# Kernel tuning notes

Hardware: AMD Instinct MI355X
Metric: run time of the kernel (lower is better)

## Reference

```python
import jax, jax.numpy as jnp
import numpy as np

B, C, S = 32, 64, 112
RATIO = 8
EPS = 1e-5


def conv1x1(x, w, b):
    # 1x1 conv == channel-mixing matmul. x:[B,C,H,W], w:[O,C], b:[O]
    return jnp.einsum('oc,bchw->bohw', w, x) + b[None, :, None, None]


def dwconv(x, w, b):
    # grouped 1x1 conv with groups=C: per-channel scale + bias
    return x * w[None, :, None, None] + b[None, :, None, None]


def bn(x, g, b):
    # BatchNorm2d in training mode: batch stats over (N,H,W), biased var
    m = x.mean((0, 2, 3), keepdims=True)
    v = x.var((0, 2, 3), keepdims=True)
    return (x - m) * jax.lax.rsqrt(v + EPS) * g[None, :, None, None] + b[None, :, None, None]


def avgpool(x, k):
    # nn.AvgPool2d(k): kernel k, stride k, VALID (floor) padding
    s = jax.lax.reduce_window(x, 0.0, jax.lax.add, (1, 1, k, k), (1, 1, k, k), 'VALID')
    return s / float(k * k)


def setup_inputs() -> dict:
    key = jax.random.key(0)
    ks = jax.random.split(key, 20)
    C2, H = 2 * C, (2 * C) // RATIO

    def n(k, shape, s=0.02):
        return jax.random.normal(k, shape, jnp.float32) * s

    return {
        'rgb': jax.random.normal(ks[0], (B, C, S, S), jnp.float32),
        'fre': jax.random.normal(ks[1], (B, C, S, S), jnp.float32),
        'wq_fad': n(ks[2], (C, C)), 'bq_fad': jnp.zeros((C,), jnp.float32),
        'wq_lfs': n(ks[3], (C, C)), 'bq_lfs': jnp.zeros((C,), jnp.float32),
        'wk_fad': n(ks[4], (C, C)), 'bk_fad': jnp.zeros((C,), jnp.float32),
        'wk_lfs': n(ks[5], (C, C)), 'bk_lfs': jnp.zeros((C,), jnp.float32),
        'fad_gamma': n(ks[6], (1,), 1.0), 'lfs_gamma': n(ks[7], (1,), 1.0),
        'fad_cw': n(ks[8], (C,), 1.0), 'fad_cb': jnp.zeros((C,), jnp.float32),
        'fad_bg': jnp.ones((C,), jnp.float32), 'fad_bb': jnp.zeros((C,), jnp.float32),
        'lfs_cw': n(ks[9], (C,), 1.0), 'lfs_cb': jnp.zeros((C,), jnp.float32),
        'lfs_bg': jnp.ones((C,), jnp.float32), 'lfs_bb': jnp.zeros((C,), jnp.float32),
        'lin1_w': n(ks[10], (3,), 0.3), 'lin2_w': n(ks[11], (3,), 0.3),
        'mlp_w1': n(ks[12], (H, C2)), 'mlp_w2': n(ks[13], (C2, H)),
        'rgb_cw': n(ks[14], (C,), 1.0), 'rgb_cb': jnp.zeros((C,), jnp.float32),
        'rgb_bg': jnp.ones((C,), jnp.float32), 'rgb_bb': jnp.zeros((C,), jnp.float32),
        'fre_cw': n(ks[15], (C,), 1.0), 'fre_cb': jnp.zeros((C,), jnp.float32),
        'fre_bg': jnp.ones((C,), jnp.float32), 'fre_bb': jnp.zeros((C,), jnp.float32),
    }


def reference(rgb, fre, wq_fad, bq_fad, wq_lfs, bq_lfs, wk_fad, bk_fad, wk_lfs, bk_lfs,
              fad_gamma, lfs_gamma, fad_cw, fad_cb, fad_bg, fad_bb,
              lfs_cw, lfs_cb, lfs_bg, lfs_bb, lin1_w, lin2_w, mlp_w1, mlp_w2,
              rgb_cw, rgb_cb, rgb_bg, rgb_bb, fre_cw, fre_cb, fre_bg, fre_bb):
    Bn, Cn, Sz, _ = rgb.shape
    # ---- MixBlock: cross attention over folded (B*C) batch ----
    qF = conv1x1(rgb, wq_fad, bq_fad).reshape(Bn * Cn, Sz, Sz)
    qL = conv1x1(fre, wq_lfs, bq_lfs).reshape(Bn * Cn, Sz, Sz)
    Mq = jnp.concatenate([qF, qL], axis=2)          # [BC, S, 2S]
    kF = conv1x1(rgb, wk_fad, bk_fad).reshape(Bn * Cn, Sz, Sz).transpose(0, 2, 1)
    kL = conv1x1(fre, wk_lfs, bk_lfs).reshape(Bn * Cn, Sz, Sz).transpose(0, 2, 1)
    Mk = jnp.concatenate([kF, kL], axis=1)          # [BC, 2S, S]
    attn = jax.nn.softmax(jnp.matmul(Mq, Mk), axis=-1).reshape(Bn, Cn, Sz, Sz)
    att_lfs = fre * attn * (jax.nn.sigmoid(lfs_gamma) * 2.0 - 1.0)
    y_fad = rgb + bn(dwconv(att_lfs, fad_cw, fad_cb), fad_bg, fad_bb)
    att_fad = rgb * attn * (jax.nn.sigmoid(fad_gamma) * 2.0 - 1.0)
    y_lfs = fre + bn(dwconv(att_fad, lfs_cw, lfs_cb), lfs_bg, lfs_bb)
    # ---- MSCA on concatenated channels ----
    x = jnp.concatenate([y_fad, y_lfs], axis=1)     # [B, 2C, S, S]
    avgs, maxs = [], []
    for k in (3, 5, 7):
        m = avgpool(x, k)
        avgs.append(m.mean((2, 3)))
        maxs.append(m.max((2, 3)))
    a_p = jnp.stack(avgs, -1) @ lin1_w              # [B, 2C]
    m_p = jnp.stack(maxs, -1) @ lin2_w

    def mlp(v):
        h = jax.nn.relu(jnp.einsum('rc,bc->br', mlp_w1, v))
        return jnp.einsum('cr,br->bc', mlp_w2, h)

    ca = jax.nn.sigmoid(mlp(a_p) + mlp(m_p))        # [B, 2C]
    r_c = ca[:, :Cn, None, None]
    f_c = ca[:, Cn:, None, None]
    rgb_out = y_fad + bn(dwconv(r_c * y_fad, rgb_cw, rgb_cb), rgb_bg, rgb_bb)
    fre_out = y_lfs + bn(dwconv(f_c * y_lfs, fre_cw, fre_cb), fre_bg, fre_bb)
    return (rgb_out, fre_out)
```

## Files before the change

kernel.cpp:

```cpp
#include <hip/hip_runtime.h>
#include <hip/hip_bf16.h>
#include <stdint.h>

#define NE 25690112ull
#define PP 12544
#define SS 112
#define EPSV 1e-5f

typedef __attribute__((ext_vector_type(8))) short short8v;
typedef __attribute__((ext_vector_type(4))) float float4v;

__device__ __forceinline__ unsigned short f2bf(float x){
  union { __hip_bfloat16 h; unsigned short u; } cv;
  cv.h = __float2bfloat16(x);
  return cv.u;
}
__device__ __forceinline__ ushort4 f2bf4(float a, float b, float c, float d){
  union { __hip_bfloat162 h2[2]; ushort4 u; } cv;
  cv.h2[0] = __float22bfloat162_rn(make_float2(a, b));
  cv.h2[1] = __float22bfloat162_rn(make_float2(c, d));
  return cv.u;
}
__device__ __forceinline__ float bf2f(unsigned short u){ return __uint_as_float(((uint32_t)u) << 16); }

__global__ __launch_bounds__(256) void k1_conv(
    const float* __restrict__ rgb, const float* __restrict__ fre,
    const float* __restrict__ wq_fad, const float* __restrict__ bq_fad,
    const float* __restrict__ wk_fad, const float* __restrict__ bk_fad,
    const float* __restrict__ wq_lfs, const float* __restrict__ bq_lfs,
    const float* __restrict__ wk_lfs, const float* __restrict__ bk_lfs,
    unsigned short* __restrict__ qF, unsigned short* __restrict__ kF,
    unsigned short* __restrict__ qL, unsigned short* __restrict__ kL)
{
  const int bx = blockIdx.x, b = blockIdx.y, z = blockIdx.z;
  const float* X  = z ? fre : rgb;
  const float* Wq = z ? wq_lfs : wq_fad;
  const float* Bq = z ? bq_lfs : bq_fad;
  const float* Wk = z ? wk_lfs : wk_fad;
  const float* Bk = z ? bk_lfs : bk_fad;
  unsigned short* Oq = z ? qL : qF;
  unsigned short* Ok = z ? kL : kF;

  __shared__ __align__(16) unsigned short xs[256 * 64];

  const int tid = threadIdx.x, lane = tid & 63, w = tid >> 6;
  const int lc = lane & 15, l4 = lane >> 4;

  const int p0 = bx*256;
  const size_t xbase = (size_t)b * 64 * PP;
  const int c0 = (tid & 15) * 4;
  const int pq = (tid >> 4) * 4;
  #pragma unroll
  for (int itp = 0; itp < 4; ++itp){
    const int p = itp*64 + pq;
    float4 xr[4];
    #pragma unroll
    for (int k = 0; k < 4; ++k)
      xr[k] = *(const float4*)(X + xbase + (size_t)(c0+k)*PP + p0 + p);
    const float* v0 = &xr[0].x;
    const float* v1 = &xr[1].x;
    const float* v2 = &xr[2].x;
    const float* v3 = &xr[3].x;
    #pragma unroll
    for (int j = 0; j < 4; ++j){
      ushort4 t = f2bf4(v0[j], v1[j], v2[j], v3[j]);
      uint32_t byteS = (uint32_t)((p+j)*128 + c0*2) ^ (uint32_t)(((p+j) & 7) << 4);
      *(ushort4*)((char*)xs + byteS) = t;
    }
  }
  __syncthreads();

  short8v afr[4][2];
  #pragma unroll
  for (int t = 0; t < 4; ++t){
    const int row = (t*4 + w)*16 + lc;
    const uint32_t rbase = (uint32_t)(row*128);
    const uint32_t sw = (uint32_t)((row & 7) << 4);
    afr[t][0] = *(const short8v*)((const char*)xs + ((rbase + l4*16) ^ sw));
    afr[t][1] = *(const short8v*)((const char*)xs + ((rbase + 64 + l4*16) ^ sw));
  }
  __syncthreads();

  #pragma unroll
  for (int arr = 0; arr < 2; ++arr){
    const float* W = arr ? Wk : Wq;
    const float* Bi = arr ? Bk : Bq;
    unsigned short* O = arr ? Ok : Oq;
    short8v wf[4][2];
    float bias[4];
    #pragma unroll
    for (int ot = 0; ot < 4; ++ot){
      bias[ot] = Bi[ot*16 + lc];
      #pragma unroll
      for (int ks = 0; ks < 2; ++ks){
        const int base = (ot*16 + lc)*64 + ks*32 + l4*8;
        const float4 q0 = *(const float4*)(W + base);
        const float4 q1 = *(const float4*)(W + base + 4);
        union { ushort4 u[2]; short8v v; } pk;
        pk.u[0] = f2bf4(q0.x, q0.y, q0.z, q0.w);
        pk.u[1] = f2bf4(q1.x, q1.y, q1.z, q1.w);
        wf[ot][ks] = pk.v;
      }
    }
    #pragma unroll
    for (int t = 0; t < 4; ++t){
      const int pt = (t*4 + w)*16;
      #pragma unroll
      for (int ot = 0; ot < 4; ++ot){
        float4v acc = (float4v){bias[ot], bias[ot], bias[ot], bias[ot]};
        acc = __builtin_amdgcn_mfma_f32_16x16x32_bf16(afr[t][0], wf[ot][0], acc, 0, 0, 0);
        acc = __builtin_amdgcn_mfma_f32_16x16x32_bf16(afr[t][1], wf[ot][1], acc, 0, 0, 0);
        ushort4 u = f2bf4(acc[0], acc[1], acc[2], acc[3]);
        const int o = ot*16 + lc;
        uint32_t byteS = (uint32_t)(o*512 + (pt + l4*4)*2) ^ (uint32_t)((o & 7) << 4);
        *(ushort4*)((char*)xs + byteS) = u;
      }
    }
    __syncthreads();
    for (int i = tid; i < 2048; i += 256){
      const int o = i >> 5, s = i & 31;
      uint32_t byteS = (uint32_t)(o*512 + s*16) ^ (uint32_t)((o & 7) << 4);
      short8v v = *(const short8v*)((const char*)xs + byteS);
      *(short8v*)(O + ((size_t)b*64 + o)*PP + p0 + s*8) = v;
    }
    __syncthreads();
  }
}

__global__ __launch_bounds__(448) void k2_attn(
    unsigned short* __restrict__ qF, const unsigned short* __restrict__ qL,
    const unsigned short* __restrict__ kF, const unsigned short* __restrict__ kL,
    const float* __restrict__ rgb, const float* __restrict__ fre,
    const float* __restrict__ fad_gamma, const float* __restrict__ lfs_gamma,
    float* __restrict__ stats)
{
  const int bc = blockIdx.x, c = bc & 63;
  const size_t plane = (size_t)bc * PP;
  __shared__ __align__(16) unsigned short ksF[PP + 16];
  __shared__ __align__(16) unsigned short ksL[PP + 16];
  const int tid = threadIdx.x, lane = tid & 63, w = tid >> 6;
  const int l4 = lane >> 4, lc = lane & 15;

  const unsigned short* qFp = qF + plane;
  const unsigned short* qLp = qL + plane;
  const int qrow = w*16 + lc;
  short8v aF[4], aL[4];
  #pragma unroll
  for (int ks = 0; ks < 4; ++ks){
    const int joff = ks*32 + l4*8;
    if ((ks < 3) || (l4 < 2)){
      aF[ks] = *(const short8v*)(qFp + qrow*SS + joff);
      aL[ks] = *(const short8v*)(qLp + qrow*SS + joff);
    } else {
      aF[ks] = (short8v)(short)0;
      aL[ks] = (short8v)(short)0;
    }
  }

  const uint32_t* kFu = (const uint32_t*)kF + plane/2;
  const uint32_t* kLu = (const uint32_t*)kL + plane/2;
  uint32_t* ksFw = (uint32_t*)ksF;
  uint32_t* ksLw = (uint32_t*)ksL;
  #pragma unroll
  for (int t = 0; t < 14; ++t){
    const int i = tid + t*448;
    ksFw[i] = kFu[i];
    ksLw[i] = kLu[i];
  }
  __syncthreads();

  float4v acc[7];
  #pragma unroll
  for (int ct = 0; ct < 7; ++ct) acc[ct] = (float4v)0.f;
  #pragma unroll
  for (int ks = 0; ks < 4; ++ks){
    #pragma unroll
    for (int ct = 0; ct < 7; ++ct){
      const uint32_t off = (uint32_t)((ct*16 + lc)*224 + ks*64 + l4*16);
      short8v bF = *(const short8v*)((const char*)ksF + off);
      short8v bL = *(const short8v*)((const char*)ksL + off);
      acc[ct] = __builtin_amdgcn_mfma_f32_16x16x32_bf16(aF[ks], bF, acc[ct], 0, 0, 0);
      acc[ct] = __builtin_amdgcn_mfma_f32_16x16x32_bf16(aL[ks], bL, acc[ct], 0, 0, 0);
    }
  }

  const float sF = 2.f/(1.f + __expf(-fad_gamma[0])) - 1.f;
  const float sL = 2.f/(1.f + __expf(-lfs_gamma[0])) - 1.f;
  unsigned short* attnP = qF + plane;
  unsigned short* alin = ksF;

  __syncthreads();
  #pragma unroll
  for (int r = 0; r < 4; ++r){
    const int i = w*16 + l4*4 + r;
    float v[7];
    #pragma unroll
    for (int ct = 0; ct < 7; ++ct) v[ct] = acc[ct][r];
    float m = fmaxf(fmaxf(fmaxf(v[0],v[1]),fmaxf(v[2],v[3])), fmaxf(fmaxf(v[4],v[5]),v[6]));
    #pragma unroll
    for (int off = 8; off; off >>= 1) m = fmaxf(m, __shfl_xor(m, off, 64));
    float e[7]; float s = 0.f;
    #pragma unroll
    for (int ct = 0; ct < 7; ++ct){ e[ct] = __expf(v[ct] - m); s += e[ct]; }
    #pragma unroll
    for (int off = 8; off; off >>= 1) s += __shfl_xor(s, off, 64);
    const float inv = 1.f / s;
    #pragma unroll
    for (int ct = 0; ct < 7; ++ct)
      alin[i*SS + ct*16 + lc] = f2bf(e[ct] * inv);
  }
  __syncthreads();

  float ls1 = 0.f, lq1 = 0.f, ls2 = 0.f, lq2 = 0.f;
  #pragma unroll
  for (int t = 0; t < 7; ++t){
    const int i4 = tid + t*448;
    ushort4 av = *(const ushort4*)(alin + i4*4);
    *(ushort4*)(attnP + (size_t)i4*4) = av;
    float4 fr = *(const float4*)(fre + plane + (size_t)i4*4);
    float4 rg = *(const float4*)(rgb + plane + (size_t)i4*4);
    const unsigned short* ap = &av.x;
    const float fp[4] = {fr.x, fr.y, fr.z, fr.w};
    const float rp[4] = {rg.x, rg.y, rg.z, rg.w};
    #pragma unroll
    for (int j = 0; j < 4; ++j){
      float a = bf2f(ap[j]);
      float v1 = fp[j] * a * sL;
      float v2 = rp[j] * a * sF;
      ls1 += v1; lq1 += v1*v1; ls2 += v2; lq2 += v2*v2;
    }
  }
  #pragma unroll
  for (int off = 32; off; off >>= 1){
    ls1 += __shfl_xor(ls1, off, 64);
    lq1 += __shfl_xor(lq1, off, 64);
    ls2 += __shfl_xor(ls2, off, 64);
    lq2 += __shfl_xor(lq2, off, 64);
  }
  if (lane == 0){
    atomicAdd(&stats[c],       ls1);
    atomicAdd(&stats[64 + c],  lq1);
    atomicAdd(&stats[128 + c], ls2);
    atomicAdd(&stats[192 + c], lq2);
  }
}

__global__ void k3_affine1(const float* __restrict__ stats,
    const float* __restrict__ fad_cw, const float* __restrict__ fad_bg, const float* __restrict__ fad_bb,
    const float* __restrict__ lfs_cw, const float* __restrict__ lfs_bg, const float* __restrict__ lfs_bb,
    float* __restrict__ AB)
{
  int c = threadIdx.x;
  if (c >= 64) return;
  const float n = 401408.f;
  {
    float m1 = stats[c]/n, v1 = stats[64+c]/n - (stats[c]/n)*(stats[c]/n);
    float cw = fad_cw[c], g = fad_bg[c];
    float rs = rsqrtf(cw*cw*v1 + EPSV);
    AB[c]      = cw*rs*g;
    AB[64 + c] = -cw*m1*rs*g + fad_bb[c];
  }
  {
    float m2 = stats[128+c]/n, v2 = stats[192+c]/n - (stats[128+c]/n)*(stats[128+c]/n);
    float cw = lfs_cw[c], g = lfs_bg[c];
    float rs = rsqrtf(cw*cw*v2 + EPSV);
    AB[128 + c] = cw*rs*g;
    AB[192 + c] = -cw*m2*rs*g + lfs_bb[c];
  }
}

__global__ __launch_bounds__(512) void k4_fuse(
    const unsigned short* __restrict__ attn,
    const float* __restrict__ rgb, const float* __restrict__ fre,
    const float* __restrict__ AB1,
    const float* __restrict__ fad_gamma, const float* __restrict__ lfs_gamma,
    float* __restrict__ avgstat, float* __restrict__ maxstat,
    float4* __restrict__ planeStats)
{
  const int bc = blockIdx.x, b = bc >> 6, c = bc & 63;
  const size_t plane = (size_t)bc * PP;
  __shared__ unsigned short ys[2][112][113];
  __shared__ float redA[8][4];
  __shared__ float redS[8], redM[8];
  const int tid = threadIdx.x, lane = tid & 63, w = tid >> 6;
  const float sF = 2.f/(1.f + __expf(-fad_gamma[0])) - 1.f;
  const float sL = 2.f/(1.f + __expf(-lfs_gamma[0])) - 1.f;
  const float A1 = AB1[c], B1 = AB1[64+c], A2 = AB1[128+c], B2 = AB1[192+c];
  float s0 = 0.f, q0 = 0.f, s1 = 0.f, q1 = 0.f;

  for (int i4 = tid; i4 < 3136; i4 += 512){
    ushort4 av = *(const ushort4*)(attn + plane + (size_t)i4*4);
    float4 rg = *(const float4*)(rgb + plane + (size_t)i4*4);
    float4 fr = *(const float4*)(fre + plane + (size_t)i4*4);
    float aa[4] = {bf2f(av.x), bf2f(av.y), bf2f(av.z), bf2f(av.w)};
    float rr[4] = {rg.x, rg.y, rg.z, rg.w};
    float ff[4] = {fr.x, fr.y, fr.z, fr.w};
    int r = i4 / 28, c0 = (i4 % 28) * 4;
    float y0[4], y1[4];
    #pragma unroll
    for (int j = 0; j < 4; ++j){
      float t1 = ff[j]*aa[j]*sL;
      float t2 = rr[j]*aa[j]*sF;
      y0[j] = rr[j] + A1*t1 + B1;
      y1[j] = ff[j] + A2*t2 + B2;
      s0 += y0[j]; q0 += y0[j]*y0[j];
      s1 += y1[j]; q1 += y1[j]*y1[j];
    }
    *(ushort4*)(&ys[0][r][c0]) = f2bf4(y0[0], y0[1], y0[2], y0[3]);
    *(ushort4*)(&ys[1][r][c0]) = f2bf4(y1[0], y1[1], y1[2], y1[3]);
  }
  #pragma unroll
  for (int off = 32; off; off >>= 1){
    s0 += __shfl_xor(s0, off, 64); q0 += __shfl_xor(q0, off, 64);
    s1 += __shfl_xor(s1, off, 64); q1 += __shfl_xor(q1, off, 64);
  }
  if (lane == 0){ redA[w][0] = s0; redA[w][1] = q0; redA[w][2] = s1; redA[w][3] = q1; }
  __syncthreads();
  if (tid == 0){
    float a0=0,a1=0,a2=0,a3=0;
    for (int i = 0; i < 8; ++i){ a0+=redA[i][0]; a1+=redA[i][1]; a2+=redA[i][2]; a3+=redA[i][3]; }
    float4 ps = {a0,a1,a2,a3};
    planeStats[bc] = ps;
  }
  __syncthreads();

  const int kk[3] = {3,5,7};
  const int gg[3] = {37,22,16};
  for (int pl = 0; pl < 2; ++pl){
    const int cc = pl*64 + c;
    for (int ki = 0; ki < 3; ++ki){
      const int k = kk[ki], g = gg[ki];
      float sumAll = 0.f, mx = -3.0e38f;
      for (int win = tid; win < g*g; win += 512){
        int wy = win / g, wx = win % g;
        float s = 0.f;
        for (int dy = 0; dy < k; ++dy)
          for (int dx = 0; dx < k; ++dx)
            s += bf2f(ys[pl][wy*k+dy][wx*k+dx]);
        sumAll += s; mx = fmaxf(mx, s);
      }
      #pragma unroll
      for (int off = 32; off; off >>= 1){
        sumAll += __shfl_xor(sumAll, off, 64);
        mx = fmaxf(mx, __shfl_xor(mx, off, 64));
      }
      if (lane == 0){ redS[w] = sumAll; redM[w] = mx; }
      __syncthreads();
      if (tid == 0){
        float st = 0.f, mt = -3.0e38f;
        for (int i = 0; i < 8; ++i){ st += redS[i]; mt = fmaxf(mt, redM[i]); }
        int idx = (b*128 + cc)*3 + ki;
        avgstat[idx] = st / (float)(k*k*g*g);
        maxstat[idx] = mt / (float)(k*k);
      }
      __syncthreads();
    }
  }
}

__global__ void k6_mlp(const float* __restrict__ avgstat, const float* __restrict__ maxstat,
    const float* __restrict__ lin1, const float* __restrict__ lin2,
    const float* __restrict__ w1, const float* __restrict__ w2,
    float* __restrict__ ca)
{
  const int b = blockIdx.x, tid = threadIdx.x;
  __shared__ float sa[128], sm[128], hA[16], hM[16];
  int idx = (b*128 + tid)*3;
  sa[tid] = avgstat[idx]*lin1[0] + avgstat[idx+1]*lin1[1] + avgstat[idx+2]*lin1[2];
  sm[tid] = maxstat[idx]*lin2[0] + maxstat[idx+1]*lin2[1] + maxstat[idx+2]*lin2[2];
  __syncthreads();
  if (tid < 16){
    float ha = 0.f, hm = 0.f;
    for (int c2 = 0; c2 < 128; ++c2){
      ha += w1[tid*128 + c2]*sa[c2];
      hm += w1[tid*128 + c2]*sm[c2];
    }
    hA[tid] = fmaxf(ha, 0.f); hM[tid] = fmaxf(hm, 0.f);
  }
  __syncthreads();
  float o = 0.f;
  for (int r = 0; r < 16; ++r) o += w2[tid*16 + r]*(hA[r] + hM[r]);
  ca[b*128 + tid] = 1.f/(1.f + __expf(-o));
}

__global__ void k8_affineF(const float4* __restrict__ planeStats, const float* __restrict__ ca,
    const float* __restrict__ rgb_cw, const float* __restrict__ rgb_bg, const float* __restrict__ rgb_bb,
    const float* __restrict__ fre_cw, const float* __restrict__ fre_bg, const float* __restrict__ fre_bb,
    float* __restrict__ ABF)
{
  int t = threadIdx.x;
  if (t >= 128) return;
  int z = t >> 6, c = t & 63;
  float S = 0.f, Q = 0.f;
  for (int b = 0; b < 32; ++b){
    float4 ps = planeStats[b*64 + c];
    float sc = ca[b*128 + t];
    float sp = z ? ps.z : ps.x;
    float qp = z ? ps.w : ps.y;
    S += sc*sp; Q += sc*sc*qp;
  }
  const float n = 401408.f;
  float m = S/n, v = Q/n - m*m;
  float cw = z ? fre_cw[c] : rgb_cw[c];
  float g  = z ? fre_bg[c] : rgb_bg[c];
  float bb = z ? fre_bb[c] : rgb_bb[c];
  float rs = rsqrtf(cw*cw*v + EPSV);
  ABF[z*128 + c]      = cw*rs*g;
  ABF[z*128 + 64 + c] = -cw*m*rs*g + bb;
}

__global__ __launch_bounds__(256) void k9_out(
    const unsigned short* __restrict__ attn,
    const float* __restrict__ rgb, const float* __restrict__ fre,
    const float* __restrict__ AB1,
    const float* __restrict__ fad_gamma, const float* __restrict__ lfs_gamma,
    const float* __restrict__ ca, const float* __restrict__ ABF,
    float* __restrict__ out)
{
  const int c = blockIdx.x, b = blockIdx.y;
  const size_t plane = ((size_t)b*64 + c)*PP;
  const float sF = 2.f/(1.f + __expf(-fad_gamma[0])) - 1.f;
  const float sL = 2.f/(1.f + __expf(-lfs_gamma[0])) - 1.f;
  const float A1 = AB1[c], B1 = AB1[64+c], A2 = AB1[128+c], B2 = AB1[192+c];
  const float r_c = ca[b*128 + c], f_c = ca[b*128 + 64 + c];
  const float mul0 = 1.f + ABF[c]*r_c,        add0 = ABF[64 + c];
  const float mul1 = 1.f + ABF[128 + c]*f_c,  add1 = ABF[192 + c];
  float* o0 = out + plane;
  float* o1 = out + NE + plane;
  for (int i4 = threadIdx.x; i4 < 3136; i4 += 256){
    ushort4 av = *(const ushort4*)(attn + plane + (size_t)i4*4);
    float4 rg = *(const float4*)(rgb + plane + (size_t)i4*4);
    float4 fr = *(const float4*)(fre + plane + (size_t)i4*4);
    float aa[4] = {bf2f(av.x), bf2f(av.y), bf2f(av.z), bf2f(av.w)};
    float rr[4] = {rg.x, rg.y, rg.z, rg.w};
    float ff[4] = {fr.x, fr.y, fr.z, fr.w};
    float4 v0, v1;
    float* p0 = &v0.x; float* p1 = &v1.x;
    #pragma unroll
    for (int j = 0; j < 4; ++j){
      float t1 = ff[j]*aa[j]*sL;
      float t2 = rr[j]*aa[j]*sF;
      float y0 = rr[j] + A1*t1 + B1;
      float y1 = ff[j] + A2*t2 + B2;
      p0[j] = y0*mul0 + add0;
      p1[j] = y1*mul1 + add1;
    }
    *(float4*)(&o0[(size_t)i4*4]) = v0;
    *(float4*)(&o1[(size_t)i4*4]) = v1;
  }
}

extern "C" void kernel_launch(void* const* d_in, const int* in_sizes, int n_in,
                              void* d_out, int out_size, void* d_ws, size_t ws_size,
                              hipStream_t stream)
{
  (void)in_sizes; (void)n_in; (void)out_size; (void)ws_size;
  const float* rgb      = (const float*)d_in[0];
  const float* fre      = (const float*)d_in[1];
  const float* wq_fad   = (const float*)d_in[2];
  const float* bq_fad   = (const float*)d_in[3];
  const float* wq_lfs   = (const float*)d_in[4];
  const float* bq_lfs   = (const float*)d_in[5];
  const float* wk_fad   = (const float*)d_in[6];
  const float* bk_fad   = (const float*)d_in[7];
  const float* wk_lfs   = (const float*)d_in[8];
  const float* bk_lfs   = (const float*)d_in[9];
  const float* fad_gamma= (const float*)d_in[10];
  const float* lfs_gamma= (const float*)d_in[11];
  const float* fad_cw   = (const float*)d_in[12];
  const float* fad_bg   = (const float*)d_in[14];
  const float* fad_bb   = (const float*)d_in[15];
  const float* lfs_cw   = (const float*)d_in[16];
  const float* lfs_bg   = (const float*)d_in[18];
  const float* lfs_bb   = (const float*)d_in[19];
  const float* lin1_w   = (const float*)d_in[20];
  const float* lin2_w   = (const float*)d_in[21];
  const float* mlp_w1   = (const float*)d_in[22];
  const float* mlp_w2   = (const float*)d_in[23];
  const float* rgb_cw   = (const float*)d_in[24];
  const float* rgb_bg   = (const float*)d_in[26];
  const float* rgb_bb   = (const float*)d_in[27];
  const float* fre_cw   = (const float*)d_in[28];
  const float* fre_bg   = (const float*)d_in[30];
  const float* fre_bb   = (const float*)d_in[31];

  char* ws = (char*)d_ws;
  unsigned short* qF = (unsigned short*)(ws);
  unsigned short* qL = (unsigned short*)(ws + 2*NE);
  unsigned short* kF = (unsigned short*)(ws + 4*NE);
  unsigned short* kL = (unsigned short*)(ws + 6*NE);
  float* sbase = (float*)(ws + 8*NE);
  float* stats      = sbase;
  float* AB1        = sbase + 256;
  float* avgstat    = sbase + 512;
  float* maxstat    = sbase + 12800;
  float* ca         = sbase + 25088;
  float* ABF        = sbase + 29184;
  float4* planeStats= (float4*)(sbase + 29440);

  hipMemsetAsync(stats, 0, 256*sizeof(float), stream);

  k1_conv<<<dim3(49,32,2), dim3(256), 0, stream>>>(rgb, fre,
      wq_fad, bq_fad, wk_fad, bk_fad, wq_lfs, bq_lfs, wk_lfs, bk_lfs,
      qF, kF, qL, kL);
  k2_attn<<<dim3(2048), dim3(448), 0, stream>>>(qF, qL, kF, kL,
      rgb, fre, fad_gamma, lfs_gamma, stats);
  k3_affine1<<<dim3(1), dim3(64), 0, stream>>>(stats,
      fad_cw, fad_bg, fad_bb, lfs_cw, lfs_bg, lfs_bb, AB1);
  k4_fuse<<<dim3(2048), dim3(512), 0, stream>>>((const unsigned short*)qF,
      rgb, fre, AB1, fad_gamma, lfs_gamma, avgstat, maxstat, planeStats);
  k6_mlp<<<dim3(32), dim3(128), 0, stream>>>(avgstat, maxstat,
      lin1_w, lin2_w, mlp_w1, mlp_w2, ca);
  k8_affineF<<<dim3(1), dim3(128), 0, stream>>>(planeStats, ca,
      rgb_cw, rgb_bg, rgb_bb, fre_cw, fre_bg, fre_bb, ABF);
  k9_out<<<dim3(64,32), dim3(256), 0, stream>>>((const unsigned short*)qF,
      rgb, fre, AB1, fad_gamma, lfs_gamma, ca, ABF, (float*)d_out);
}
```

Baseline: 403.3 us.

## Store K in channel-interleaved tiled layout and read it directly from global

The conv kernel now writes K tensors in a layout tiled by 16 pixels with all 64 channels interleaved, directly from MFMA registers, without the shared-memory transpose. The attention kernel no longer stages the K plane into LDS; it loads B fragments straight from global memory. This frees one of the two LDS buffers, which may raise occupancy, and removes a sync and a copy. In exchange the global loads are more scattered, each a 16-byte chunk at a 2KB stride across channels, so cache efficiency may suffer.

```diff
diff --git a/kernel.cpp b/kernel.cpp
--- a/kernel.cpp
+++ b/kernel.cpp
@@ -6,6 +6,7 @@
 #define PP 12544
 #define SS 112
 #define EPSV 1e-5f
+#define BSTR 802816
 
 typedef __attribute__((ext_vector_type(8))) short short8v;
 typedef __attribute__((ext_vector_type(4))) float float4v;
@@ -29,8 +30,8 @@
     const float* __restrict__ wk_fad, const float* __restrict__ bk_fad,
     const float* __restrict__ wq_lfs, const float* __restrict__ bq_lfs,
     const float* __restrict__ wk_lfs, const float* __restrict__ bk_lfs,
-    unsigned short* __restrict__ qF, unsigned short* __restrict__ kF,
-    unsigned short* __restrict__ qL, unsigned short* __restrict__ kL)
+    unsigned short* __restrict__ qF, unsigned short* __restrict__ kFt,
+    unsigned short* __restrict__ qL, unsigned short* __restrict__ kLt)
 {
   const int bx = blockIdx.x, b = blockIdx.y, z = blockIdx.z;
   const float* X  = z ? fre : rgb;
@@ -39,7 +40,7 @@
   const float* Wk = z ? wk_lfs : wk_fad;
   const float* Bk = z ? bk_lfs : bk_fad;
   unsigned short* Oq = z ? qL : qF;
-  unsigned short* Ok = z ? kL : kF;
+  unsigned short* Ok = z ? kLt : kFt;
 
   __shared__ __align__(16) unsigned short xs[256 * 64];
 
@@ -81,21 +82,17 @@
   }
   __syncthreads();
 
-  #pragma unroll
-  for (int arr = 0; arr < 2; ++arr){
-    const float* W = arr ? Wk : Wq;
-    const float* Bi = arr ? Bk : Bq;
-    unsigned short* O = arr ? Ok : Oq;
+  {
     short8v wf[4][2];
     float bias[4];
     #pragma unroll
     for (int ot = 0; ot < 4; ++ot){
-      bias[ot] = Bi[ot*16 + lc];
+      bias[ot] = Bq[ot*16 + lc];
       #pragma unroll
       for (int ks = 0; ks < 2; ++ks){
         const int base = (ot*16 + lc)*64 + ks*32 + l4*8;
-        const float4 q0 = *(const float4*)(W + base);
-        const float4 q1 = *(const float4*)(W + base + 4);
+        const float4 q0 = *(const float4*)(Wq + base);
+        const float4 q1 = *(const float4*)(Wq + base + 4);
         union { ushort4 u[2]; short8v v; } pk;
         pk.u[0] = f2bf4(q0.x, q0.y, q0.z, q0.w);
         pk.u[1] = f2bf4(q1.x, q1.y, q1.z, q1.w);
@@ -121,23 +118,54 @@
       const int o = i >> 5, s = i & 31;
       uint32_t byteS = (uint32_t)(o*512 + s*16) ^ (uint32_t)((o & 7) << 4);
       short8v v = *(const short8v*)((const char*)xs + byteS);
-      *(short8v*)(O + ((size_t)b*64 + o)*PP + p0 + s*8) = v;
-    }
-    __syncthreads();
+      *(short8v*)(Oq + ((size_t)b*64 + o)*PP + p0 + s*8) = v;
+    }
+  }
+
+  {
+    short8v wf[4][2];
+    float bias[4];
+    #pragma unroll
+    for (int ot = 0; ot < 4; ++ot){
+      bias[ot] = Bk[ot*16 + lc];
+      #pragma unroll
+      for (int ks = 0; ks < 2; ++ks){
+        const int base = (ot*16 + lc)*64 + ks*32 + l4*8;
+        const float4 q0 = *(const float4*)(Wk + base);
+        const float4 q1 = *(const float4*)(Wk + base + 4);
+        union { ushort4 u[2]; short8v v; } pk;
+        pk.u[0] = f2bf4(q0.x, q0.y, q0.z, q0.w);
+        pk.u[1] = f2bf4(q1.x, q1.y, q1.z, q1.w);
+        wf[ot][ks] = pk.v;
+      }
+    }
+    unsigned short* Okb = Ok + (size_t)b * BSTR;
+    #pragma unroll
+    for (int t = 0; t < 4; ++t){
+      const int p16 = bx*16 + t*4 + w;
+      #pragma unroll
+      for (int ot = 0; ot < 4; ++ot){
+        float4v acc = (float4v){bias[ot], bias[ot], bias[ot], bias[ot]};
+        acc = __builtin_amdgcn_mfma_f32_16x16x32_bf16(afr[t][0], wf[ot][0], acc, 0, 0, 0);
+        acc = __builtin_amdgcn_mfma_f32_16x16x32_bf16(afr[t][1], wf[ot][1], acc, 0, 0, 0);
+        ushort4 u = f2bf4(acc[0], acc[1], acc[2], acc[3]);
+        const int o = ot*16 + lc;
+        *(ushort4*)(Okb + (size_t)p16*1024 + o*16 + l4*4) = u;
+      }
+    }
   }
 }
 
 __global__ __launch_bounds__(448) void k2_attn(
     unsigned short* __restrict__ qF, const unsigned short* __restrict__ qL,
-    const unsigned short* __restrict__ kF, const unsigned short* __restrict__ kL,
+    const unsigned short* __restrict__ kFt, const unsigned short* __restrict__ kLt,
     const float* __restrict__ rgb, const float* __restrict__ fre,
     const float* __restrict__ fad_gamma, const float* __restrict__ lfs_gamma,
     float* __restrict__ stats)
 {
-  const int bc = blockIdx.x, c = bc & 63;
+  const int bc = blockIdx.x, c = bc & 63, b = bc >> 6;
   const size_t plane = (size_t)bc * PP;
-  __shared__ __align__(16) unsigned short ksF[PP + 16];
-  __shared__ __align__(16) unsigned short ksL[PP + 16];
+  __shared__ __align__(16) unsigned short alin[PP + 16];
   const int tid = threadIdx.x, lane = tid & 63, w = tid >> 6;
   const int l4 = lane >> 4, lc = lane & 15;
 
@@ -157,28 +185,21 @@
     }
   }
 
-  const uint32_t* kFu = (const uint32_t*)kF + plane/2;
-  const uint32_t* kLu = (const uint32_t*)kL + plane/2;
-  uint32_t* ksFw = (uint32_t*)ksF;
-  uint32_t* ksLw = (uint32_t*)ksL;
-  #pragma unroll
-  for (int t = 0; t < 14; ++t){
-    const int i = tid + t*448;
-    ksFw[i] = kFu[i];
-    ksLw[i] = kLu[i];
-  }
-  __syncthreads();
-
+  const unsigned short* kFb = kFt + (size_t)b * BSTR;
+  const unsigned short* kLb = kLt + (size_t)b * BSTR;
   float4v acc[7];
   #pragma unroll
   for (int ct = 0; ct < 7; ++ct) acc[ct] = (float4v)0.f;
   #pragma unroll
   for (int ks = 0; ks < 4; ++ks){
+    const int j = ks*32 + l4*8;
+    const int jj = (j < 112) ? j : 0;
     #pragma unroll
     for (int ct = 0; ct < 7; ++ct){
-      const uint32_t off = (uint32_t)((ct*16 + lc)*224 + ks*64 + l4*16);
-      short8v bF = *(const short8v*)((const char*)ksF + off);
-      short8v bL = *(const short8v*)((const char*)ksL + off);
+      const int p = (ct*16 + lc)*SS + jj;
+      const uint32_t idx = (uint32_t)(p >> 4)*1024u + (uint32_t)(c*16 + (p & 15));
+      short8v bF = *(const short8v*)(kFb + idx);
+      short8v bL = *(const short8v*)(kLb + idx);
       acc[ct] = __builtin_amdgcn_mfma_f32_16x16x32_bf16(aF[ks], bF, acc[ct], 0, 0, 0);
       acc[ct] = __builtin_amdgcn_mfma_f32_16x16x32_bf16(aL[ks], bL, acc[ct], 0, 0, 0);
     }
@@ -187,9 +208,7 @@
   const float sF = 2.f/(1.f + __expf(-fad_gamma[0])) - 1.f;
   const float sL = 2.f/(1.f + __expf(-lfs_gamma[0])) - 1.f;
   unsigned short* attnP = qF + plane;
-  unsigned short* alin = ksF;
-
-  __syncthreads();
+
   #pragma unroll
   for (int r = 0; r < 4; ++r){
     const int i = w*16 + l4*4 + r;
@@ -485,10 +504,10 @@
   const float* fre_bb   = (const float*)d_in[31];
 
   char* ws = (char*)d_ws;
-  unsigned short* qF = (unsigned short*)(ws);
-  unsigned short* qL = (unsigned short*)(ws + 2*NE);
-  unsigned short* kF = (unsigned short*)(ws + 4*NE);
-  unsigned short* kL = (unsigned short*)(ws + 6*NE);
+  unsigned short* qF  = (unsigned short*)(ws);
+  unsigned short* qL  = (unsigned short*)(ws + 2*NE);
+  unsigned short* kFt = (unsigned short*)(ws + 4*NE);
+  unsigned short* kLt = (unsigned short*)(ws + 6*NE);
   float* sbase = (float*)(ws + 8*NE);
   float* stats      = sbase;
   float* AB1        = sbase + 256;
@@ -502,8 +521,8 @@
 
   k1_conv<<<dim3(49,32,2), dim3(256), 0, stream>>>(rgb, fre,
       wq_fad, bq_fad, wk_fad, bk_fad, wq_lfs, bq_lfs, wk_lfs, bk_lfs,
-      qF, kF, qL, kL);
-  k2_attn<<<dim3(2048), dim3(448), 0, stream>>>(qF, qL, kF, kL,
+      qF, kFt, qL, kLt);
+  k2_attn<<<dim3(2048), dim3(448), 0, stream>>>(qF, qL, kFt, kLt,
       rgb, fre, fad_gamma, lfs_gamma, stats);
   k3_affine1<<<dim3(1), dim3(64), 0, stream>>>(stats,
       fad_cw, fad_bg, fad_bb, lfs_cw, lfs_bg, lfs_bb, AB1);
```

Measured after the change: 560.1 us. 1.39x slower.
